# Kernel optimization log

Measured on AMD Instinct MI355X. Metric: run time of the kernel, lower is better.

The kernel has to match this reference:

```python
import jax, jax.numpy as jnp
import numpy as np

B, F_DIM, P, C, H = 16, 256, 8192, 96, 256


def setup_inputs() -> dict:
    key = jax.random.key(0)
    ks = jax.random.split(key, 8)
    seg_feat = jax.random.normal(ks[0], (B, F_DIM, P), dtype=jnp.float32)
    seg_label = jax.random.randint(ks[1], (B, P), 0, C, dtype=jnp.int64 if jax.config.read('jax_enable_x64') else jnp.int32)
    s1 = 1.0 / np.sqrt(F_DIM)
    s2 = 1.0 / np.sqrt(H)
    w1 = jax.random.uniform(ks[2], (F_DIM, H), jnp.float32, -s1, s1)
    b1 = jax.random.uniform(ks[3], (H,), jnp.float32, -s1, s1)
    w2 = jax.random.uniform(ks[4], (H, H), jnp.float32, -s2, s2)
    b2 = jax.random.uniform(ks[5], (H,), jnp.float32, -s2, s2)
    w_logit = jax.random.uniform(ks[6], (H, C), jnp.float32, -s2, s2)
    b_logit = jax.random.uniform(ks[7], (C,), jnp.float32, -s2, s2)
    return dict(seg_feat=seg_feat, seg_label=seg_label, w1=w1, b1=b1,
                w2=w2, b2=b2, w_logit=w_logit, b_logit=b_logit)


def _pool_by_class(seg_feat, seg_label, num_classes):
    # seg_feat: [B, F, P], seg_label: [B, P] -> pooled [B*C, F]
    b, f, p = seg_feat.shape
    seg_ids = (jnp.arange(b, dtype=seg_label.dtype)[:, None] * num_classes
               + seg_label).reshape(-1)                       # [B*P]
    feat = seg_feat.transpose(0, 2, 1).reshape(b * p, f)      # [B*P, F]
    segmax = jax.ops.segment_max(feat, seg_ids, num_segments=b * num_classes)
    counts = jax.ops.segment_sum(jnp.ones((b * p,), feat.dtype), seg_ids,
                                 num_segments=b * num_classes)  # [B*C]
    counts = counts[:, None]
    # torch: max over points of feat * onehot -> zeros from other classes
    # participate in the max unless the class covers ALL points; empty
    # classes pool to 0 (max of all zeros).
    pooled = jnp.where(counts == 0, 0.0,
                       jnp.where(counts == p, segmax, jnp.maximum(segmax, 0.0)))
    return pooled


def reference(seg_feat, seg_label, w1, b1, w2, b2, w_logit, b_logit):
    num_classes = w_logit.shape[1]
    pooled = _pool_by_class(seg_feat, seg_label, num_classes)   # [B*C, F]
    # feat_mlp: Linear+ReLU x2 (dropout_prob=0), then part_logit
    h = jax.nn.relu(pooled @ w1 + b1)
    h = jax.nn.relu(h @ w2 + b2)
    part_pred = h @ w_logit + b_logit                           # [B*C, C]
    b = seg_feat.shape[0]
    part_batch = jnp.repeat(jnp.arange(b), num_classes)
    part_label = jnp.tile(jnp.arange(num_classes), b)
    return part_pred, part_label, part_batch
```

## Files before the change

### kernel.cpp

```cpp
#include <hip/hip_runtime.h>

#define B 16
#define F_DIM 256
#define P 8192
#define C 96
#define H 256
#define NSEG (B * C)
#define G 8
#define NFBLK (F_DIM / G)
#define SPLIT 4
#define PQ (P / SPLIT)


__global__ __launch_bounds__(256) void pool_kernel(const float* __restrict__ feat,
                                                   const int* __restrict__ label,
                                                   int* __restrict__ kbuf,
                                                   int* __restrict__ cnts) {
    __shared__ int smax[G][C];
    __shared__ int hist[C];
    const int blk = blockIdx.x;
    const int q  = blk & 3;
    const int fg = (blk >> 2) & 31;
    const int b  = blk >> 7;
    const int f0 = fg << 3;
    const int t = threadIdx.x;

    for (int i = t; i < G * C; i += 256) ((int*)smax)[i] = 0x80000000;
    if (t < C) hist[t] = 0;
    __syncthreads();

    const int4* lrow4 = (const int4*)(label + (size_t)b * P + (size_t)q * PQ);
    int4 lab[2];
    lab[0] = lrow4[t];
    lab[1] = lrow4[t + 256];

    if (fg == 0) {
        #pragma unroll
        for (int j = 0; j < 2; ++j) {
            atomicAdd(&hist[lab[j].x], 1);
            atomicAdd(&hist[lab[j].y], 1);
            atomicAdd(&hist[lab[j].z], 1);
            atomicAdd(&hist[lab[j].w], 1);
        }
    }

    const float4* fbase4 = (const float4*)(feat + ((size_t)b * F_DIM + f0) * P + (size_t)q * PQ);

    float4 cur[2], nxt[2];
    cur[0] = fbase4[t];
    cur[1] = fbase4[t + 256];

    #pragma unroll
    for (int f = 0; f < G; ++f) {
        if (f + 1 < G) {
            nxt[0] = fbase4[(size_t)(f + 1) * (P / 4) + t];
            nxt[1] = fbase4[(size_t)(f + 1) * (P / 4) + t + 256];
        }
        #pragma unroll
        for (int j = 0; j < 2; ++j) {
            atomicMax(&smax[f][lab[j].x], __float_as_int(cur[j].x));
            atomicMax(&smax[f][lab[j].y], __float_as_int(cur[j].y));
            atomicMax(&smax[f][lab[j].z], __float_as_int(cur[j].z));
            atomicMax(&smax[f][lab[j].w], __float_as_int(cur[j].w));
        }
        cur[0] = nxt[0];
        cur[1] = nxt[1];
    }
    __syncthreads();

    if (fg == 0 && t < C) cnts[q * NSEG + b * C + t] = hist[t];

    if (t < C) {
        int4 lo, hi;
        lo.x = smax[0][t]; lo.y = smax[1][t]; lo.z = smax[2][t]; lo.w = smax[3][t];
        hi.x = smax[4][t]; hi.y = smax[5][t]; hi.z = smax[6][t]; hi.w = smax[7][t];
        int* dst = kbuf + (size_t)q * NSEG * F_DIM + (size_t)(b * C + t) * F_DIM + f0;
        *(int4*)dst = lo;
        *(int4*)(dst + 4) = hi;
    }
}

__global__ __launch_bounds__(256, 3) void dense1_kernel(const int* __restrict__ kx,
                                                        const int* __restrict__ cnts,
                                                        const float* __restrict__ w,
                                                        const float* __restrict__ bias,
                                                        float* __restrict__ y) {
    constexpr int COLS = 64;
    __shared__ float xs[8][H];
    __shared__ float ps[8][COLS][17];
    const int t = threadIdx.x;
    const int row0 = blockIdx.x * 8;
    const int bj0 = blockIdx.y * COLS;

    {
        const int4* k4 = (const int4*)kx;
        const size_t base = (size_t)row0 * (H / 4);
        #pragma unroll
        for (int jj = 0; jj < 2; ++jj) {
            const int i = t + jj * 256;
            int4 km = k4[base + i];
            #pragma unroll
            for (int h = 1; h < SPLIT; ++h) {
                const int4 kh = k4[(size_t)h * NSEG * (H / 4) + base + i];
                km.x = km.x > kh.x ? km.x : kh.x;
                km.y = km.y > kh.y ? km.y : kh.y;
                km.z = km.z > kh.z ? km.z : kh.z;
                km.w = km.w > kh.w ? km.w : kh.w;
            }
            const int row = row0 + (i >> 6);
            const int cnt = cnts[row] + cnts[NSEG + row] +
                            cnts[2 * NSEG + row] + cnts[3 * NSEG + row];
            float4 v;
            v.x = __int_as_float(km.x); v.y = __int_as_float(km.y);
            v.z = __int_as_float(km.z); v.w = __int_as_float(km.w);
            if (cnt == 0) {
                v.x = v.y = v.z = v.w = 0.0f;
            } else if (cnt != P) {
                v.x = fmaxf(v.x, 0.0f); v.y = fmaxf(v.y, 0.0f);
                v.z = fmaxf(v.z, 0.0f); v.w = fmaxf(v.w, 0.0f);
            }
            ((float4*)xs)[i] = v;
        }
    }
    __syncthreads();

    const int s = t >> 4;
    const int jq = t & 15;

    {
        const float4* w4 = (const float4*)w;
        const int wq = (bj0 >> 2) + jq;
        const int kbase = s * 16;
        float4 acc[8];
        #pragma unroll
        for (int r = 0; r < 8; ++r) acc[r] = (float4){0.f, 0.f, 0.f, 0.f};

        #pragma unroll
        for (int i = 0; i < 16; ++i) {
            const int k = kbase + i;
            const float4 wv = w4[k * (H / 4) + wq];
            #pragma unroll
            for (int r = 0; r < 8; ++r) {
                const float xv = xs[r][k];
                acc[r].x = fmaf(xv, wv.x, acc[r].x);
                acc[r].y = fmaf(xv, wv.y, acc[r].y);
                acc[r].z = fmaf(xv, wv.z, acc[r].z);
                acc[r].w = fmaf(xv, wv.w, acc[r].w);
            }
        }
        #pragma unroll
        for (int r = 0; r < 8; ++r) {
            ps[r][jq * 4 + 0][s] = acc[r].x;
            ps[r][jq * 4 + 1][s] = acc[r].y;
            ps[r][jq * 4 + 2][s] = acc[r].z;
            ps[r][jq * 4 + 3][s] = acc[r].w;
        }
    }
    __syncthreads();

    for (int e = t; e < 8 * COLS; e += 256) {
        const int r = e / COLS, j = e % COLS;
        float v = bias[bj0 + j];
        #pragma unroll
        for (int qq = 0; qq < 16; ++qq) v += ps[r][j][qq];
        y[(size_t)(row0 + r) * H + bj0 + j] = fmaxf(v, 0.0f);
    }
}

__global__ __launch_bounds__(256, 2) void dense23_kernel(const float* __restrict__ h1,
                                                         const float* __restrict__ w2,
                                                         const float* __restrict__ b2,
                                                         const float* __restrict__ wl,
                                                         const float* __restrict__ bl,
                                                         float* __restrict__ out,
                                                         float* __restrict__ tails) {
    __shared__ float xs[8][H];
    __shared__ float xs2[8][H];
    __shared__ float ps[8][H][5];
    float (*ps2)[C][3] = (float(*)[C][3])ps;
    const int t = threadIdx.x;
    const int row0 = blockIdx.x * 8;

    ((float4*)xs)[t]       = ((const float4*)(h1 + (size_t)row0 * H))[t];
    ((float4*)xs)[t + 256] = ((const float4*)(h1 + (size_t)row0 * H))[t + 256];
    __syncthreads();

    {
        const int jq = t & 63;
        const int s  = t >> 6;
        const float4* w4 = (const float4*)w2;
        const int kbase = s * 64;
        float4 acc[8];
        #pragma unroll
        for (int r = 0; r < 8; ++r) acc[r] = (float4){0.f, 0.f, 0.f, 0.f};

        #pragma unroll 8
        for (int i = 0; i < 64; ++i) {
            const int k = kbase + i;
            const float4 wv = w4[k * (H / 4) + jq];
            #pragma unroll
            for (int r = 0; r < 8; ++r) {
                const float xv = xs[r][k];
                acc[r].x = fmaf(xv, wv.x, acc[r].x);
                acc[r].y = fmaf(xv, wv.y, acc[r].y);
                acc[r].z = fmaf(xv, wv.z, acc[r].z);
                acc[r].w = fmaf(xv, wv.w, acc[r].w);
            }
        }
        #pragma unroll
        for (int r = 0; r < 8; ++r) {
            ps[r][jq * 4 + 0][s] = acc[r].x;
            ps[r][jq * 4 + 1][s] = acc[r].y;
            ps[r][jq * 4 + 2][s] = acc[r].z;
            ps[r][jq * 4 + 3][s] = acc[r].w;
        }
    }
    __syncthreads();

    #pragma unroll
    for (int e = t; e < 8 * H; e += 256) {
        const int r = e >> 8, j = e & 255;
        float v = b2[j] + ps[r][j][0] + ps[r][j][1] + ps[r][j][2] + ps[r][j][3];
        xs2[r][j] = fmaxf(v, 0.0f);
    }
    __syncthreads();

    if (t < 192) {
        const int half = t / C;
        const int j = t - half * C;
        const int kbase = half * 128;
        float acc[8];
        #pragma unroll
        for (int r = 0; r < 8; ++r) acc[r] = 0.0f;
        #pragma unroll 8
        for (int i = 0; i < 128; ++i) {
            const int k = kbase + i;
            const float wv = wl[k * C + j];
            #pragma unroll
            for (int r = 0; r < 8; ++r) acc[r] = fmaf(xs2[r][k], wv, acc[r]);
        }
        #pragma unroll
        for (int r = 0; r < 8; ++r) ps2[r][j][half] = acc[r];
    }
    __syncthreads();

    for (int e = t; e < 8 * C; e += 256) {
        const int r = e / C, j = e % C;
        out[(size_t)(row0 + r) * C + j] = bl[j] + ps2[r][j][0] + ps2[r][j][1];
    }

    if (t < 8) {
        const int row = row0 + t;
        tails[row] = (float)(row % C);
        tails[NSEG + row] = (float)(row / C);
    }
}

extern "C" void kernel_launch(void* const* d_in, const int* in_sizes, int n_in,
                              void* d_out, int out_size, void* d_ws, size_t ws_size,
                              hipStream_t stream) {
    const float* feat  = (const float*)d_in[0];
    const int*   label = (const int*)d_in[1];
    const float* w1    = (const float*)d_in[2];
    const float* b1    = (const float*)d_in[3];
    const float* w2    = (const float*)d_in[4];
    const float* b2    = (const float*)d_in[5];
    const float* wl    = (const float*)d_in[6];
    const float* bl    = (const float*)d_in[7];
    float* out = (float*)d_out;

    char* ws = (char*)d_ws;
    const size_t KBYTES = (size_t)SPLIT * NSEG * H * 4;
    int*   kbuf = (int*)ws;
    int*   cnts = (int*)(ws + KBYTES);
    float* h1   = (float*)(ws + KBYTES + 32768);

    pool_kernel<<<B * NFBLK * SPLIT, 256, 0, stream>>>(feat, label, kbuf, cnts);
    dense1_kernel<<<dim3(NSEG / 8, 4), 256, 0, stream>>>(kbuf, cnts, w1, b1, h1);
    dense23_kernel<<<NSEG / 8, 256, 0, stream>>>(h1, w2, b2, wl, bl, out, out + (size_t)NSEG * C);
}
```

Measured before the change: 48.60 us.

## Fuse dense MLP layers into one kernel with per-group atomic spin barriers

```diff
diff --git a/kernel.cpp b/kernel.cpp
--- a/kernel.cpp
+++ b/kernel.cpp
@@ -10,12 +10,14 @@
 #define NFBLK (F_DIM / G)
 #define SPLIT 4
 #define PQ (P / SPLIT)
+#define NGRP (NSEG / 8)
 
 
 __global__ __launch_bounds__(256) void pool_kernel(const float* __restrict__ feat,
                                                    const int* __restrict__ label,
                                                    int* __restrict__ kbuf,
-                                                   int* __restrict__ cnts) {
+                                                   int* __restrict__ cnts,
+                                                   int* __restrict__ flags) {
     __shared__ int smax[G][C];
     __shared__ int hist[C];
     const int blk = blockIdx.x;
@@ -25,6 +27,10 @@
     const int f0 = fg << 3;
     const int t = threadIdx.x;
 
+    if (blk == 0) {
+        for (int i = t; i < 2 * NGRP; i += 256) flags[i] = 0;
+    }
+
     for (int i = t; i < G * C; i += 256) ((int*)smax)[i] = 0x80000000;
     if (t < C) hist[t] = 0;
     __syncthreads();
@@ -80,17 +86,35 @@
     }
 }
 
-__global__ __launch_bounds__(256, 3) void dense1_kernel(const int* __restrict__ kx,
-                                                        const int* __restrict__ cnts,
-                                                        const float* __restrict__ w,
-                                                        const float* __restrict__ bias,
-                                                        float* __restrict__ y) {
-    constexpr int COLS = 64;
+__device__ __forceinline__ void spin4(int* p) {
+    int it = 0;
+    while (__hip_atomic_load(p, __ATOMIC_ACQUIRE, __HIP_MEMORY_SCOPE_AGENT) != 4) {
+        __builtin_amdgcn_s_sleep(8);
+        if (++it > (1 << 20)) break;
+    }
+}
+
+__global__ __launch_bounds__(256, 3) void fused_mlp(const int* __restrict__ kx,
+                                                    const int* __restrict__ cnts,
+                                                    const float* __restrict__ w1,
+                                                    const float* __restrict__ b1,
+                                                    const float* __restrict__ w2,
+                                                    const float* __restrict__ b2,
+                                                    const float* __restrict__ wl,
+                                                    const float* __restrict__ bl,
+                                                    float* __restrict__ h1,
+                                                    float* __restrict__ h2,
+                                                    float* __restrict__ out,
+                                                    int* __restrict__ done1,
+                                                    int* __restrict__ done2) {
     __shared__ float xs[8][H];
-    __shared__ float ps[8][COLS][17];
+    __shared__ float ps[8][64][17];
     const int t = threadIdx.x;
-    const int row0 = blockIdx.x * 8;
-    const int bj0 = blockIdx.y * COLS;
+    const int grp = blockIdx.x >> 2;
+    const int j = blockIdx.x & 3;
+    const int row0 = grp * 8;
+    const int s = t >> 4;
+    const int jq = t & 15;
 
     {
         const int4* k4 = (const int4*)kx;
@@ -123,18 +147,14 @@
         }
     }
     __syncthreads();
-
-    const int s = t >> 4;
-    const int jq = t & 15;
-
-    {
-        const float4* w4 = (const float4*)w;
+    {
+        const int bj0 = 64 * j;
+        const float4* w4 = (const float4*)w1;
         const int wq = (bj0 >> 2) + jq;
         const int kbase = s * 16;
         float4 acc[8];
         #pragma unroll
         for (int r = 0; r < 8; ++r) acc[r] = (float4){0.f, 0.f, 0.f, 0.f};
-
         #pragma unroll
         for (int i = 0; i < 16; ++i) {
             const int k = kbase + i;
@@ -157,47 +177,36 @@
         }
     }
     __syncthreads();
-
-    for (int e = t; e < 8 * COLS; e += 256) {
-        const int r = e / COLS, j = e % COLS;
-        float v = bias[bj0 + j];
-        #pragma unroll
-        for (int qq = 0; qq < 16; ++qq) v += ps[r][j][qq];
-        y[(size_t)(row0 + r) * H + bj0 + j] = fmaxf(v, 0.0f);
-    }
-}
-
-__global__ __launch_bounds__(256, 2) void dense23_kernel(const float* __restrict__ h1,
-                                                         const float* __restrict__ w2,
-                                                         const float* __restrict__ b2,
-                                                         const float* __restrict__ wl,
-                                                         const float* __restrict__ bl,
-                                                         float* __restrict__ out,
-                                                         float* __restrict__ tails) {
-    __shared__ float xs[8][H];
-    __shared__ float xs2[8][H];
-    __shared__ float ps[8][H][5];
-    float (*ps2)[C][3] = (float(*)[C][3])ps;
-    const int t = threadIdx.x;
-    const int row0 = blockIdx.x * 8;
+    {
+        const int bj0 = 64 * j;
+        for (int e = t; e < 8 * 64; e += 256) {
+            const int r = e >> 6, c = e & 63;
+            float v = b1[bj0 + c];
+            #pragma unroll
+            for (int qq = 0; qq < 16; ++qq) v += ps[r][c][qq];
+            h1[(size_t)(row0 + r) * H + bj0 + c] = fmaxf(v, 0.0f);
+        }
+    }
+    __syncthreads();
+    if (t == 0) __hip_atomic_fetch_add(&done1[grp], 1, __ATOMIC_RELEASE, __HIP_MEMORY_SCOPE_AGENT);
+    spin4(&done1[grp]);
+    __syncthreads();
 
     ((float4*)xs)[t]       = ((const float4*)(h1 + (size_t)row0 * H))[t];
     ((float4*)xs)[t + 256] = ((const float4*)(h1 + (size_t)row0 * H))[t + 256];
     __syncthreads();
-
-    {
-        const int jq = t & 63;
-        const int s  = t >> 6;
+    {
+        const int bj0 = 64 * j;
         const float4* w4 = (const float4*)w2;
-        const int kbase = s * 64;
+        const int wq = (bj0 >> 2) + jq;
+        const int kbase = s * 16;
         float4 acc[8];
         #pragma unroll
         for (int r = 0; r < 8; ++r) acc[r] = (float4){0.f, 0.f, 0.f, 0.f};
-
-        #pragma unroll 8
-        for (int i = 0; i < 64; ++i) {
+        #pragma unroll
+        for (int i = 0; i < 16; ++i) {
             const int k = kbase + i;
-            const float4 wv = w4[k * (H / 4) + jq];
+            const float4 wv = w4[k * (H / 4) + wq];
             #pragma unroll
             for (int r = 0; r < 8; ++r) {
                 const float xv = xs[r][k];
@@ -216,43 +225,71 @@
         }
     }
     __syncthreads();
-
-    #pragma unroll
-    for (int e = t; e < 8 * H; e += 256) {
-        const int r = e >> 8, j = e & 255;
-        float v = b2[j] + ps[r][j][0] + ps[r][j][1] + ps[r][j][2] + ps[r][j][3];
-        xs2[r][j] = fmaxf(v, 0.0f);
-    }
-    __syncthreads();
-
-    if (t < 192) {
-        const int half = t / C;
-        const int j = t - half * C;
-        const int kbase = half * 128;
-        float acc[8];
-        #pragma unroll
-        for (int r = 0; r < 8; ++r) acc[r] = 0.0f;
-        #pragma unroll 8
-        for (int i = 0; i < 128; ++i) {
-            const int k = kbase + i;
-            const float wv = wl[k * C + j];
-            #pragma unroll
-            for (int r = 0; r < 8; ++r) acc[r] = fmaf(xs2[r][k], wv, acc[r]);
-        }
-        #pragma unroll
-        for (int r = 0; r < 8; ++r) ps2[r][j][half] = acc[r];
-    }
-    __syncthreads();
-
-    for (int e = t; e < 8 * C; e += 256) {
-        const int r = e / C, j = e % C;
-        out[(size_t)(row0 + r) * C + j] = bl[j] + ps2[r][j][0] + ps2[r][j][1];
-    }
-
-    if (t < 8) {
-        const int row = row0 + t;
-        tails[row] = (float)(row % C);
-        tails[NSEG + row] = (float)(row / C);
+    {
+        const int bj0 = 64 * j;
+        for (int e = t; e < 8 * 64; e += 256) {
+            const int r = e >> 6, c = e & 63;
+            float v = b2[bj0 + c];
+            #pragma unroll
+            for (int qq = 0; qq < 16; ++qq) v += ps[r][c][qq];
+            h2[(size_t)(row0 + r) * H + bj0 + c] = fmaxf(v, 0.0f);
+        }
+    }
+    __syncthreads();
+    if (t == 0) __hip_atomic_fetch_add(&done2[grp], 1, __ATOMIC_RELEASE, __HIP_MEMORY_SCOPE_AGENT);
+    if (j >= 2) return;
+    spin4(&done2[grp]);
+    __syncthreads();
+
+    ((float4*)xs)[t]       = ((const float4*)(h2 + (size_t)row0 * H))[t];
+    ((float4*)xs)[t + 256] = ((const float4*)(h2 + (size_t)row0 * H))[t + 256];
+    __syncthreads();
+    {
+        const int bj0 = 48 * j;
+        if (jq < 12) {
+            const float4* w4 = (const float4*)wl;
+            const int wq = (bj0 >> 2) + jq;
+            const int kbase = s * 16;
+            float4 acc[8];
+            #pragma unroll
+            for (int r = 0; r < 8; ++r) acc[r] = (float4){0.f, 0.f, 0.f, 0.f};
+            #pragma unroll
+            for (int i = 0; i < 16; ++i) {
+                const int k = kbase + i;
+                const float4 wv = w4[k * (C / 4) + wq];
+                #pragma unroll
+                for (int r = 0; r < 8; ++r) {
+                    const float xv = xs[r][k];
+                    acc[r].x = fmaf(xv, wv.x, acc[r].x);
+                    acc[r].y = fmaf(xv, wv.y, acc[r].y);
+                    acc[r].z = fmaf(xv, wv.z, acc[r].z);
+                    acc[r].w = fmaf(xv, wv.w, acc[r].w);
+                }
+            }
+            #pragma unroll
+            for (int r = 0; r < 8; ++r) {
+                ps[r][jq * 4 + 0][s] = acc[r].x;
+                ps[r][jq * 4 + 1][s] = acc[r].y;
+                ps[r][jq * 4 + 2][s] = acc[r].z;
+                ps[r][jq * 4 + 3][s] = acc[r].w;
+            }
+        }
+    }
+    __syncthreads();
+    {
+        const int bj0 = 48 * j;
+        for (int e = t; e < 8 * 48; e += 256) {
+            const int r = e / 48, c = e % 48;
+            float v = bl[bj0 + c];
+            #pragma unroll
+            for (int qq = 0; qq < 16; ++qq) v += ps[r][c][qq];
+            out[(size_t)(row0 + r) * C + bj0 + c] = v;
+        }
+        if (j == 0 && t < 8) {
+            const int row = row0 + t;
+            out[(size_t)NSEG * C + row] = (float)(row % C);
+            out[(size_t)NSEG * C + NSEG + row] = (float)(row / C);
+        }
     }
 }
 
@@ -271,11 +308,13 @@
 
     char* ws = (char*)d_ws;
     const size_t KBYTES = (size_t)SPLIT * NSEG * H * 4;
-    int*   kbuf = (int*)ws;
-    int*   cnts = (int*)(ws + KBYTES);
-    float* h1   = (float*)(ws + KBYTES + 32768);
-
-    pool_kernel<<<B * NFBLK * SPLIT, 256, 0, stream>>>(feat, label, kbuf, cnts);
-    dense1_kernel<<<dim3(NSEG / 8, 4), 256, 0, stream>>>(kbuf, cnts, w1, b1, h1);
-    dense23_kernel<<<NSEG / 8, 256, 0, stream>>>(h1, w2, b2, wl, bl, out, out + (size_t)NSEG * C);
+    int*   kbuf  = (int*)ws;
+    int*   cnts  = (int*)(ws + KBYTES);
+    int*   flags = (int*)(ws + KBYTES + 32768);
+    float* h1    = (float*)(ws + KBYTES + 65536);
+    float* h2    = (float*)(ws + KBYTES + 65536 + (size_t)NSEG * H * 4);
+
+    pool_kernel<<<B * NFBLK * SPLIT, 256, 0, stream>>>(feat, label, kbuf, cnts, flags);
+    fused_mlp<<<NGRP * 4, 256, 0, stream>>>(kbuf, cnts, w1, b1, w2, b2, wl, bl,
+                                            h1, h2, out, flags, flags + NGRP);
 }
```

New measurement: 176.4 us. 3.63x slower.
